# Kernel tuning notes

Measured on AMD Instinct MI355X. Metric: run time of the kernel, lower is better.

The kernel has to match this reference:

```python
import jax, jax.numpy as jnp
import numpy as np

MARGIN = 0.8
EPS = 1e-6  # torch F.pairwise_distance eps added to the difference


def setup_inputs() -> dict:
    key = jax.random.key(0)
    k1, k2, k3 = jax.random.split(key, 3)
    B, D = 8192, 128
    emb = jax.random.normal(k1, (B, D), dtype=jnp.float32)
    labels = jax.random.randint(k2, (B,), 0, 6)
    sbj = jax.random.randint(k3, (B,), 0, 16)
    return {"emb": emb, "labels": labels, "sbj": sbj}


def reference(emb, labels, sbj):
    B = emb.shape[0]
    # Squared pairwise distances (monotone in true distance -> same argmax/argmin)
    sq = jnp.sum(emb * emb, axis=1)
    d2 = sq[:, None] + sq[None, :] - 2.0 * (emb @ emb.T)  # [B, B]
    same_s = sbj[:, None] == sbj[None, :]
    same_l = labels[:, None] == labels[None, :]
    eye = jnp.eye(B, dtype=bool)
    pos_m = same_s & same_l & ~eye          # within-subject, same label, not self
    neg_m = same_s & ~same_l                # within-subject, different label
    valid = pos_m.any(axis=1) & neg_m.any(axis=1)
    p_idx = jnp.argmax(jnp.where(pos_m, d2, -jnp.inf), axis=1)  # hardest positive
    n_idx = jnp.argmin(jnp.where(neg_m, d2, jnp.inf), axis=1)   # hardest negative
    # TripletMarginLoss(p=2): pairwise_distance adds eps to the difference
    dap = jnp.linalg.norm(emb - emb[p_idx] + EPS, axis=1)
    dan = jnp.linalg.norm(emb - emb[n_idx] + EPS, axis=1)
    per = jnp.maximum(dap - dan + MARGIN, 0.0)
    cnt = jnp.sum(valid)
    loss = jnp.sum(jnp.where(valid, per, 0.0)) / jnp.maximum(cnt, 1)
    return jnp.where(cnt > 0, loss, 0.0)
```

## Files before the change

### kernel.cpp

```cpp
#include <hip/hip_runtime.h>
#include <math.h>
#include <limits.h>

#define D 128
#define NSUBJ 16
#define MAXN 640
#define MARGIN 0.8f
#define PRB 32
#define NPB 256
#define TI 16
#define TJ 64
#define NSTRIPE 32
#define NBLK (NSUBJ * NSTRIPE)

typedef __attribute__((ext_vector_type(8))) short bf16x8;
typedef __attribute__((ext_vector_type(4))) float f32x4;

static __device__ __forceinline__ short f2bf(float f) {
    union { float f; unsigned u; } v; v.f = f;
    unsigned r = v.u + 0x7FFF + ((v.u >> 16) & 1);
    return (short)(r >> 16);
}

__global__ __launch_bounds__(64) void hist_kernel(const int* __restrict__ sbj,
                                                  int* __restrict__ hist) {
    __shared__ int s_cnt[NSUBJ];
    const int t = threadIdx.x, bid = blockIdx.x;
    if (t < NSUBJ) s_cnt[t] = 0;
    __syncthreads();
    if (t < PRB) atomicAdd(&s_cnt[sbj[bid * PRB + t]], 1);
    __syncthreads();
    if (t < NSUBJ) hist[bid * NSUBJ + t] = s_cnt[t];
}

__global__ __launch_bounds__(256) void prep_kernel(
        const float* __restrict__ emb, const int* __restrict__ labels,
        const int* __restrict__ sbj, const int* __restrict__ hist,
        int* __restrict__ counts,
        int4* __restrict__ pmeta, short* __restrict__ ebf, int B) {
    __shared__ int s_cnt[NSUBJ], s_base[NSUBJ], s_slot[PRB];
    const int t = threadIdx.x, bid = blockIdx.x;
    if (t < NSUBJ) { s_cnt[t] = 0; s_base[t] = 0; }
    __syncthreads();
    {
        const int ss = t & 15, seg0 = (t >> 4) * 16;
        int part = 0;
        const int hi = min(bid, seg0 + 16);
        for (int b = seg0; b < hi; ++b) part += hist[b * NSUBJ + ss];
        if (part) atomicAdd(&s_base[ss], part);
    }
    int s = 0, mypos = 0;
    if (t < PRB) { s = sbj[bid * PRB + t]; mypos = atomicAdd(&s_cnt[s], 1); }
    __syncthreads();
    if (t < PRB) {
        int pos = s_base[s] + mypos;
        s_slot[t] = (pos < MAXN) ? (s * MAXN + pos) : -1;
    }
    if (bid == NPB - 1 && t < NSUBJ)
        counts[t] = s_base[t] + s_cnt[t];
    __syncthreads();
#pragma unroll
    for (int it = 0; it < (PRB * 16) / 256; ++it) {
        int lin = it * 256 + t;
        int row = lin >> 4, u = lin & 15;
        int i = bid * PRB + row;
        int slot = s_slot[row];
        const float4* rp = (const float4*)(emb + (size_t)i * D);
        float4 a0 = rp[u * 2], a1 = rp[u * 2 + 1];
        float ssq = 0.f;
        ssq = fmaf(a0.x, a0.x, ssq); ssq = fmaf(a0.y, a0.y, ssq);
        ssq = fmaf(a0.z, a0.z, ssq); ssq = fmaf(a0.w, a0.w, ssq);
        ssq = fmaf(a1.x, a1.x, ssq); ssq = fmaf(a1.y, a1.y, ssq);
        ssq = fmaf(a1.z, a1.z, ssq); ssq = fmaf(a1.w, a1.w, ssq);
#pragma unroll
        for (int off = 8; off > 0; off >>= 1) ssq += __shfl_down(ssq, off, 16);
        if (slot >= 0) {
            bf16x8 pk;
            pk[0] = f2bf(a0.x); pk[1] = f2bf(a0.y); pk[2] = f2bf(a0.z); pk[3] = f2bf(a0.w);
            pk[4] = f2bf(a1.x); pk[5] = f2bf(a1.y); pk[6] = f2bf(a1.z); pk[7] = f2bf(a1.w);
            *(bf16x8*)&ebf[(size_t)slot * D + u * 8] = pk;
            if (u == 0)
                pmeta[slot] = make_int4(labels[i], i, __float_as_int(ssq), 0);
        }
    }
}

#define LOADTILE(B0, B1, B2, B3, MI, ML, MS, JT)                         \
    do {                                                                 \
        int jl_ = (JT) * TJ + w * 16 + c, cl_ = min(jl_, n - 1);         \
        const short* rp_ = ebf + (size_t)(base + cl_) * D;               \
        B0 = *(const bf16x8*)&rp_[q * 8];                                \
        B1 = *(const bf16x8*)&rp_[32 + q * 8];                           \
        B2 = *(const bf16x8*)&rp_[64 + q * 8];                           \
        B3 = *(const bf16x8*)&rp_[96 + q * 8];                           \
        int4 m_ = pmeta[base + cl_];                                     \
        MI = (jl_ < n) ? m_.y : -1; ML = m_.x; MS = __int_as_float(m_.z);\
    } while (0)

#define STEP(B0, B1, B2, B3, MI, ML, MS)                                 \
    do {                                                                 \
        f32x4 acc = {0.f, 0.f, 0.f, 0.f};                                \
        acc = __builtin_amdgcn_mfma_f32_16x16x32_bf16(afr[0], B0, acc, 0, 0, 0); \
        acc = __builtin_amdgcn_mfma_f32_16x16x32_bf16(afr[1], B1, acc, 0, 0, 0); \
        acc = __builtin_amdgcn_mfma_f32_16x16x32_bf16(afr[2], B2, acc, 0, 0, 0); \
        acc = __builtin_amdgcn_mfma_f32_16x16x32_bf16(afr[3], B3, acc, 0, 0, 0); \
        if ((MI) >= 0) {                                                 \
            _Pragma("unroll")                                            \
            for (int r = 0; r < 4; ++r) {                                \
                float v = fmaf(-2.f, acc[r], (MS));                      \
                if ((ML) == li[r]) {                                     \
                    if ((MI) != gI[r] && v > vP[r]) { vP[r] = v; iP[r] = (MI); } \
                } else if (v < vN[r]) { vN[r] = v; iN[r] = (MI); }       \
            }                                                            \
        }                                                                \
    } while (0)

__global__ __launch_bounds__(256, 2) void triplet_kernel(
        const short* __restrict__ ebf, const int4* __restrict__ pmeta,
        const int* __restrict__ counts,
        float* __restrict__ bsum, int* __restrict__ bcnt) {
    const int bid = blockIdx.x, t = threadIdx.x;
    const int s = bid & 15;
    const int stripe = bid >> 4;
    const int base = s * MAXN;
    const int n = min(counts[s], MAXN);
    const int lane = t & 63, w = t >> 6, c = lane & 15, q = lane >> 4;

    __shared__ float svP[TI][4]; __shared__ int siP[TI][4];
    __shared__ float svN[TI][4]; __shared__ int siN[TI][4];

    float blockSum = 0.f; int blockCnt = 0;

    for (int i0 = stripe * TI; i0 < n; i0 += NSTRIPE * TI) {
        const int nrows = min(TI, n - i0);

        bf16x8 afr[4];
        {
            const short* ap = ebf + (size_t)(base + i0 + min(c, nrows - 1)) * D;
#pragma unroll
            for (int st = 0; st < 4; ++st)
                afr[st] = *(const bf16x8*)&ap[st * 32 + q * 8];
        }
        int li[4], gI[4];
#pragma unroll
        for (int r = 0; r < 4; ++r) {
            int row = q * 4 + r;
            if (row < nrows) { int4 m = pmeta[base + i0 + row]; li[r] = m.x; gI[r] = m.y; }
            else             { li[r] = INT_MIN; gI[r] = -1; }
        }

        float vP[4], vN[4]; int iP[4], iN[4];
#pragma unroll
        for (int r = 0; r < 4; ++r) {
            vP[r] = -INFINITY; iP[r] = -1;
            vN[r] =  INFINITY; iN[r] = -1;
        }

        const int ntiles = (n + TJ - 1) / TJ;
        bf16x8 b00, b01, b02, b03, b10, b11, b12, b13;
        bf16x8 b20, b21, b22, b23, b30, b31, b32, b33;
        int mi0 = -1, ml0 = INT_MIN, mi1 = -1, ml1 = INT_MIN;
        int mi2 = -1, ml2 = INT_MIN, mi3 = -1, ml3 = INT_MIN;
        float ms0 = 0.f, ms1 = 0.f, ms2 = 0.f, ms3 = 0.f;
        if (0 < ntiles) LOADTILE(b00, b01, b02, b03, mi0, ml0, ms0, 0);
        if (1 < ntiles) LOADTILE(b10, b11, b12, b13, mi1, ml1, ms1, 1);
        if (2 < ntiles) LOADTILE(b20, b21, b22, b23, mi2, ml2, ms2, 2);
        if (3 < ntiles) LOADTILE(b30, b31, b32, b33, mi3, ml3, ms3, 3);

        for (int jt = 0; jt < ntiles; jt += 4) {
            {
                bf16x8 c0 = b00, c1 = b01, c2 = b02, c3 = b03;
                int cmi = mi0, cml = ml0; float cms = ms0;
                if (jt + 4 < ntiles) LOADTILE(b00, b01, b02, b03, mi0, ml0, ms0, jt + 4);
                STEP(c0, c1, c2, c3, cmi, cml, cms);
            }
            if (jt + 1 < ntiles) {
                bf16x8 c0 = b10, c1 = b11, c2 = b12, c3 = b13;
                int cmi = mi1, cml = ml1; float cms = ms1;
                if (jt + 5 < ntiles) LOADTILE(b10, b11, b12, b13, mi1, ml1, ms1, jt + 5);
                STEP(c0, c1, c2, c3, cmi, cml, cms);
            }
            if (jt + 2 < ntiles) {
                bf16x8 c0 = b20, c1 = b21, c2 = b22, c3 = b23;
                int cmi = mi2, cml = ml2; float cms = ms2;
                if (jt + 6 < ntiles) LOADTILE(b20, b21, b22, b23, mi2, ml2, ms2, jt + 6);
                STEP(c0, c1, c2, c3, cmi, cml, cms);
            }
            if (jt + 3 < ntiles) {
                bf16x8 c0 = b30, c1 = b31, c2 = b32, c3 = b33;
                int cmi = mi3, cml = ml3; float cms = ms3;
                if (jt + 7 < ntiles) LOADTILE(b30, b31, b32, b33, mi3, ml3, ms3, jt + 7);
                STEP(c0, c1, c2, c3, cmi, cml, cms);
            }
        }

#pragma unroll
        for (int off = 8; off > 0; off >>= 1) {
#pragma unroll
            for (int r = 0; r < 4; ++r) {
                float ov = __shfl_down(vP[r], off, 16);
                int   oi = __shfl_down(iP[r], off, 16);
                if (ov > vP[r] || (ov == vP[r] && (unsigned)oi < (unsigned)iP[r])) {
                    vP[r] = ov; iP[r] = oi;
                }
                float on = __shfl_down(vN[r], off, 16);
                int   oj = __shfl_down(iN[r], off, 16);
                if (on < vN[r] || (on == vN[r] && (unsigned)oj < (unsigned)iN[r])) {
                    vN[r] = on; iN[r] = oj;
                }
            }
        }
        if (c == 0) {
#pragma unroll
            for (int r = 0; r < 4; ++r) {
                int row = q * 4 + r;
                svP[row][w] = vP[r]; siP[row][w] = iP[r];
                svN[row][w] = vN[r]; siN[row][w] = iN[r];
            }
        }
        __syncthreads();

        if (t < TI) {
            float bp = svP[t][0]; int ip = siP[t][0];
            float bn = svN[t][0]; int in_ = siN[t][0];
#pragma unroll
            for (int ww = 1; ww < 4; ++ww) {
                float o = svP[t][ww]; int oi = siP[t][ww];
                if (o > bp || (o == bp && (unsigned)oi < (unsigned)ip)) { bp = o; ip = oi; }
                float on = svN[t][ww]; int oj = siN[t][ww];
                if (on < bn || (on == bn && (unsigned)oj < (unsigned)in_)) { bn = on; in_ = oj; }
            }
            bool valid = (t < nrows) && (ip >= 0) && (in_ >= 0);
            float sqi = __int_as_float(pmeta[base + i0 + min(t, nrows - 1)].z);
            float per = 0.f;
            if (valid) {
                float dap = sqrtf(fmaxf(bp + sqi, 0.f));
                float dan = sqrtf(fmaxf(bn + sqi, 0.f));
                per = fmaxf(dap - dan + MARGIN, 0.f);
            }
            int vc = valid ? 1 : 0;
#pragma unroll
            for (int off = 8; off > 0; off >>= 1) {
                per += __shfl_down(per, off, 16);
                vc  += __shfl_down(vc,  off, 16);
            }
            if (t == 0) { blockSum += per; blockCnt += vc; }
        }
        if (i0 + NSTRIPE * TI < n) __syncthreads();
    }

    if (t == 0) { bsum[bid] = blockSum; bcnt[bid] = blockCnt; }
}

__global__ __launch_bounds__(256) void finalize_kernel(
        const float* __restrict__ bsum, const int* __restrict__ bcnt,
        float* __restrict__ out) {
    __shared__ float ssum[4]; __shared__ int scnt[4];
    const int t = threadIdx.x;
    float s = 0.f; int c = 0;
#pragma unroll
    for (int i = t; i < NBLK; i += 256) { s += bsum[i]; c += bcnt[i]; }
#pragma unroll
    for (int off = 32; off > 0; off >>= 1) {
        s += __shfl_down(s, off, 64);
        c += __shfl_down(c, off, 64);
    }
    if ((t & 63) == 0) { ssum[t >> 6] = s; scnt[t >> 6] = c; }
    __syncthreads();
    if (t == 0) {
        float S = ssum[0] + ssum[1] + ssum[2] + ssum[3];
        int   C = scnt[0] + scnt[1] + scnt[2] + scnt[3];
        out[0] = (C > 0) ? (S / (float)C) : 0.0f;
    }
}

extern "C" void kernel_launch(void* const* d_in, const int* in_sizes, int n_in,
                              void* d_out, int out_size, void* d_ws, size_t ws_size,
                              hipStream_t stream) {
    const float* emb    = (const float*)d_in[0];
    const int*   labels = (const int*)d_in[1];
    const int*   sbj    = (const int*)d_in[2];
    float*       out    = (float*)d_out;
    int B = in_sizes[1];

    char*  ws        = (char*)d_ws;
    int*   counts    = (int*)ws;
    float* bsum      = (float*)(ws + 256);
    int*   bcnt      = (int*)(ws + 256 + NBLK * sizeof(float));
    int*   hist      = (int*)(ws + 256 + 2 * NBLK * sizeof(int));
    size_t pmeta_off = (256 + 2 * (size_t)NBLK * sizeof(int)
                        + (size_t)NPB * NSUBJ * sizeof(int) + 255) & ~(size_t)255;
    int4*  pmeta     = (int4*)(ws + pmeta_off);
    size_t ebf_off   = (pmeta_off + (size_t)NSUBJ * MAXN * sizeof(int4) + 255) & ~(size_t)255;
    short* ebf       = (short*)(ws + ebf_off);

    hist_kernel<<<B / PRB, 64, 0, stream>>>(sbj, hist);
    prep_kernel<<<B / PRB, 256, 0, stream>>>(emb, labels, sbj, hist, counts,
                                             pmeta, ebf, B);
    triplet_kernel<<<NBLK, 256, 0, stream>>>(ebf, pmeta, counts, bsum, bcnt);
    finalize_kernel<<<1, 256, 0, stream>>>(bsum, bcnt, out);
}
```

Baseline: 91.61 us.

## Split column tiles across two blocks per row stripe and merge partial argmax/argmin in finalize

After: 112.8 us. 23.1% more time.

```diff
diff --git a/kernel.cpp b/kernel.cpp
--- a/kernel.cpp
+++ b/kernel.cpp
@@ -11,7 +11,9 @@
 #define TI 16
 #define TJ 64
 #define NSTRIPE 32
-#define NBLK (NSUBJ * NSTRIPE)
+#define NSPLIT 2
+#define NBLK (NSUBJ * NSTRIPE * NSPLIT)
+#define HROWS (NSUBJ * MAXN)
 
 typedef __attribute__((ext_vector_type(8))) short bf16x8;
 typedef __attribute__((ext_vector_type(4))) float f32x4;
@@ -115,13 +117,13 @@
         }                                                                \
     } while (0)
 
-__global__ __launch_bounds__(256, 2) void triplet_kernel(
+__global__ __launch_bounds__(256, 4) void triplet_kernel(
         const short* __restrict__ ebf, const int4* __restrict__ pmeta,
-        const int* __restrict__ counts,
-        float* __restrict__ bsum, int* __restrict__ bcnt) {
+        const int* __restrict__ counts, float4* __restrict__ parr) {
     const int bid = blockIdx.x, t = threadIdx.x;
     const int s = bid & 15;
-    const int stripe = bid >> 4;
+    const int stripe = (bid >> 4) & 31;
+    const int h = bid >> 9;
     const int base = s * MAXN;
     const int n = min(counts[s], MAXN);
     const int lane = t & 63, w = t >> 6, c = lane & 15, q = lane >> 4;
@@ -129,7 +131,10 @@
     __shared__ float svP[TI][4]; __shared__ int siP[TI][4];
     __shared__ float svN[TI][4]; __shared__ int siN[TI][4];
 
-    float blockSum = 0.f; int blockCnt = 0;
+    const int nt  = (n + TJ - 1) / TJ;
+    const int nt0 = (nt + 1) >> 1;
+    const int jt0 = h ? nt0 : 0;
+    const int jte = h ? nt : nt0;
 
     for (int i0 = stripe * TI; i0 < n; i0 += NSTRIPE * TI) {
         const int nrows = min(TI, n - i0);
@@ -156,40 +161,23 @@
             vN[r] =  INFINITY; iN[r] = -1;
         }
 
-        const int ntiles = (n + TJ - 1) / TJ;
         bf16x8 b00, b01, b02, b03, b10, b11, b12, b13;
-        bf16x8 b20, b21, b22, b23, b30, b31, b32, b33;
         int mi0 = -1, ml0 = INT_MIN, mi1 = -1, ml1 = INT_MIN;
-        int mi2 = -1, ml2 = INT_MIN, mi3 = -1, ml3 = INT_MIN;
-        float ms0 = 0.f, ms1 = 0.f, ms2 = 0.f, ms3 = 0.f;
-        if (0 < ntiles) LOADTILE(b00, b01, b02, b03, mi0, ml0, ms0, 0);
-        if (1 < ntiles) LOADTILE(b10, b11, b12, b13, mi1, ml1, ms1, 1);
-        if (2 < ntiles) LOADTILE(b20, b21, b22, b23, mi2, ml2, ms2, 2);
-        if (3 < ntiles) LOADTILE(b30, b31, b32, b33, mi3, ml3, ms3, 3);
-
-        for (int jt = 0; jt < ntiles; jt += 4) {
+        float ms0 = 0.f, ms1 = 0.f;
+        if (jt0 < jte)     LOADTILE(b00, b01, b02, b03, mi0, ml0, ms0, jt0);
+        if (jt0 + 1 < jte) LOADTILE(b10, b11, b12, b13, mi1, ml1, ms1, jt0 + 1);
+
+        for (int jt = jt0; jt < jte; jt += 2) {
             {
                 bf16x8 c0 = b00, c1 = b01, c2 = b02, c3 = b03;
                 int cmi = mi0, cml = ml0; float cms = ms0;
-                if (jt + 4 < ntiles) LOADTILE(b00, b01, b02, b03, mi0, ml0, ms0, jt + 4);
+                if (jt + 2 < jte) LOADTILE(b00, b01, b02, b03, mi0, ml0, ms0, jt + 2);
                 STEP(c0, c1, c2, c3, cmi, cml, cms);
             }
-            if (jt + 1 < ntiles) {
+            if (jt + 1 < jte) {
                 bf16x8 c0 = b10, c1 = b11, c2 = b12, c3 = b13;
                 int cmi = mi1, cml = ml1; float cms = ms1;
-                if (jt + 5 < ntiles) LOADTILE(b10, b11, b12, b13, mi1, ml1, ms1, jt + 5);
-                STEP(c0, c1, c2, c3, cmi, cml, cms);
-            }
-            if (jt + 2 < ntiles) {
-                bf16x8 c0 = b20, c1 = b21, c2 = b22, c3 = b23;
-                int cmi = mi2, cml = ml2; float cms = ms2;
-                if (jt + 6 < ntiles) LOADTILE(b20, b21, b22, b23, mi2, ml2, ms2, jt + 6);
-                STEP(c0, c1, c2, c3, cmi, cml, cms);
-            }
-            if (jt + 3 < ntiles) {
-                bf16x8 c0 = b30, c1 = b31, c2 = b32, c3 = b33;
-                int cmi = mi3, cml = ml3; float cms = ms3;
-                if (jt + 7 < ntiles) LOADTILE(b30, b31, b32, b33, mi3, ml3, ms3, jt + 7);
+                if (jt + 3 < jte) LOADTILE(b10, b11, b12, b13, mi1, ml1, ms1, jt + 3);
                 STEP(c0, c1, c2, c3, cmi, cml, cms);
             }
         }
@@ -230,47 +218,64 @@
                 float on = svN[t][ww]; int oj = siN[t][ww];
                 if (on < bn || (on == bn && (unsigned)oj < (unsigned)in_)) { bn = on; in_ = oj; }
             }
-            bool valid = (t < nrows) && (ip >= 0) && (in_ >= 0);
-            float sqi = __int_as_float(pmeta[base + i0 + min(t, nrows - 1)].z);
-            float per = 0.f;
-            if (valid) {
+            if (t < nrows) {
+                float4 v;
+                v.x = bp; v.y = __int_as_float(ip);
+                v.z = bn; v.w = __int_as_float(in_);
+                parr[(size_t)h * HROWS + base + i0 + t] = v;
+            }
+        }
+        if (i0 + NSTRIPE * TI < n) __syncthreads();
+    }
+}
+
+__global__ __launch_bounds__(1024) void finalize_kernel(
+        const float4* __restrict__ parr, const int4* __restrict__ pmeta,
+        const int* __restrict__ counts, float* __restrict__ out) {
+    __shared__ float fs[16]; __shared__ int fc[16];
+    const int t = threadIdx.x;
+    float sum = 0.f; int cnt = 0;
+    for (int s = 0; s < NSUBJ; ++s) {
+        const int ns = min(counts[s], MAXN);
+        for (int r = t; r < ns; r += 1024) {
+            const int slot = s * MAXN + r;
+            float4 a = parr[slot];
+            float4 b = parr[HROWS + slot];
+            float bp = a.x; int ip = __float_as_int(a.y);
+            {
+                float o = b.x; int oi = __float_as_int(b.z == b.z ? b.y : b.y);
+                oi = __float_as_int(b.y);
+                if (o > bp || (o == bp && (unsigned)oi < (unsigned)ip)) { bp = o; ip = oi; }
+            }
+            float bn = a.z; int in_ = __float_as_int(a.w);
+            {
+                float o = b.z; int oi = __float_as_int(b.w);
+                if (o < bn || (o == bn && (unsigned)oi < (unsigned)in_)) { bn = o; in_ = oi; }
+            }
+            if (ip >= 0 && in_ >= 0) {
+                float sqi = __int_as_float(pmeta[slot].z);
                 float dap = sqrtf(fmaxf(bp + sqi, 0.f));
                 float dan = sqrtf(fmaxf(bn + sqi, 0.f));
-                per = fmaxf(dap - dan + MARGIN, 0.f);
-            }
-            int vc = valid ? 1 : 0;
-#pragma unroll
-            for (int off = 8; off > 0; off >>= 1) {
-                per += __shfl_down(per, off, 16);
-                vc  += __shfl_down(vc,  off, 16);
-            }
-            if (t == 0) { blockSum += per; blockCnt += vc; }
-        }
-        if (i0 + NSTRIPE * TI < n) __syncthreads();
-    }
-
-    if (t == 0) { bsum[bid] = blockSum; bcnt[bid] = blockCnt; }
-}
-
-__global__ __launch_bounds__(256) void finalize_kernel(
-        const float* __restrict__ bsum, const int* __restrict__ bcnt,
-        float* __restrict__ out) {
-    __shared__ float ssum[4]; __shared__ int scnt[4];
-    const int t = threadIdx.x;
-    float s = 0.f; int c = 0;
-#pragma unroll
-    for (int i = t; i < NBLK; i += 256) { s += bsum[i]; c += bcnt[i]; }
+                sum += fmaxf(dap - dan + MARGIN, 0.f);
+                cnt += 1;
+            }
+        }
+    }
 #pragma unroll
     for (int off = 32; off > 0; off >>= 1) {
-        s += __shfl_down(s, off, 64);
-        c += __shfl_down(c, off, 64);
-    }
-    if ((t & 63) == 0) { ssum[t >> 6] = s; scnt[t >> 6] = c; }
-    __syncthreads();
-    if (t == 0) {
-        float S = ssum[0] + ssum[1] + ssum[2] + ssum[3];
-        int   C = scnt[0] + scnt[1] + scnt[2] + scnt[3];
-        out[0] = (C > 0) ? (S / (float)C) : 0.0f;
+        sum += __shfl_down(sum, off, 64);
+        cnt += __shfl_down(cnt, off, 64);
+    }
+    if ((t & 63) == 0) { fs[t >> 6] = sum; fc[t >> 6] = cnt; }
+    __syncthreads();
+    if (t < 16) {
+        float s2 = fs[t]; int c2 = fc[t];
+#pragma unroll
+        for (int off = 8; off > 0; off >>= 1) {
+            s2 += __shfl_down(s2, off, 16);
+            c2 += __shfl_down(c2, off, 16);
+        }
+        if (t == 0) out[0] = (c2 > 0) ? (s2 / (float)c2) : 0.0f;
     }
 }
 
@@ -285,18 +290,17 @@
 
     char*  ws        = (char*)d_ws;
     int*   counts    = (int*)ws;
-    float* bsum      = (float*)(ws + 256);
-    int*   bcnt      = (int*)(ws + 256 + NBLK * sizeof(float));
-    int*   hist      = (int*)(ws + 256 + 2 * NBLK * sizeof(int));
-    size_t pmeta_off = (256 + 2 * (size_t)NBLK * sizeof(int)
-                        + (size_t)NPB * NSUBJ * sizeof(int) + 255) & ~(size_t)255;
+    int*   hist      = (int*)(ws + 256);
+    size_t parr_off  = (256 + (size_t)NPB * NSUBJ * sizeof(int) + 255) & ~(size_t)255;
+    float4* parr     = (float4*)(ws + parr_off);
+    size_t pmeta_off = (parr_off + 2 * (size_t)HROWS * sizeof(float4) + 255) & ~(size_t)255;
     int4*  pmeta     = (int4*)(ws + pmeta_off);
-    size_t ebf_off   = (pmeta_off + (size_t)NSUBJ * MAXN * sizeof(int4) + 255) & ~(size_t)255;
+    size_t ebf_off   = (pmeta_off + (size_t)HROWS * sizeof(int4) + 255) & ~(size_t)255;
     short* ebf       = (short*)(ws + ebf_off);
 
     hist_kernel<<<B / PRB, 64, 0, stream>>>(sbj, hist);
     prep_kernel<<<B / PRB, 256, 0, stream>>>(emb, labels, sbj, hist, counts,
                                              pmeta, ebf, B);
-    triplet_kernel<<<NBLK, 256, 0, stream>>>(ebf, pmeta, counts, bsum, bcnt);
-    finalize_kernel<<<1, 256, 0, stream>>>(bsum, bcnt, out);
-}
+    triplet_kernel<<<NBLK, 256, 0, stream>>>(ebf, pmeta, counts, parr);
+    finalize_kernel<<<1, 1024, 0, stream>>>(parr, pmeta, counts, out);
+}
```

## Fuse final reduction into triplet kernel with flag-based cross-block wait

Applied to the files above, without the earlier changes.

New measurement: 93.04 us. Within noise of the previous version (+1.6%).

```diff
diff --git a/kernel.cpp b/kernel.cpp
--- a/kernel.cpp
+++ b/kernel.cpp
@@ -36,10 +36,11 @@
 __global__ __launch_bounds__(256) void prep_kernel(
         const float* __restrict__ emb, const int* __restrict__ labels,
         const int* __restrict__ sbj, const int* __restrict__ hist,
-        int* __restrict__ counts,
+        int* __restrict__ counts, int* __restrict__ bcnt,
         int4* __restrict__ pmeta, short* __restrict__ ebf, int B) {
     __shared__ int s_cnt[NSUBJ], s_base[NSUBJ], s_slot[PRB];
     const int t = threadIdx.x, bid = blockIdx.x;
+    if (t < 2) bcnt[bid * 2 + t] = 0;
     if (t < NSUBJ) { s_cnt[t] = 0; s_base[t] = 0; }
     __syncthreads();
     {
@@ -118,7 +119,8 @@
 __global__ __launch_bounds__(256, 2) void triplet_kernel(
         const short* __restrict__ ebf, const int4* __restrict__ pmeta,
         const int* __restrict__ counts,
-        float* __restrict__ bsum, int* __restrict__ bcnt) {
+        float* __restrict__ bsum, int* __restrict__ bcnt,
+        float* __restrict__ out) {
     const int bid = blockIdx.x, t = threadIdx.x;
     const int s = bid & 15;
     const int stripe = bid >> 4;
@@ -128,6 +130,7 @@
 
     __shared__ float svP[TI][4]; __shared__ int siP[TI][4];
     __shared__ float svN[TI][4]; __shared__ int siN[TI][4];
+    __shared__ float fsum[4]; __shared__ int fcnt[4];
 
     float blockSum = 0.f; int blockCnt = 0;
 
@@ -249,28 +252,37 @@
         if (i0 + NSTRIPE * TI < n) __syncthreads();
     }
 
-    if (t == 0) { bsum[bid] = blockSum; bcnt[bid] = blockCnt; }
-}
-
-__global__ __launch_bounds__(256) void finalize_kernel(
-        const float* __restrict__ bsum, const int* __restrict__ bcnt,
-        float* __restrict__ out) {
-    __shared__ float ssum[4]; __shared__ int scnt[4];
-    const int t = threadIdx.x;
-    float s = 0.f; int c = 0;
-#pragma unroll
-    for (int i = t; i < NBLK; i += 256) { s += bsum[i]; c += bcnt[i]; }
-#pragma unroll
-    for (int off = 32; off > 0; off >>= 1) {
-        s += __shfl_down(s, off, 64);
-        c += __shfl_down(c, off, 64);
-    }
-    if ((t & 63) == 0) { ssum[t >> 6] = s; scnt[t >> 6] = c; }
-    __syncthreads();
     if (t == 0) {
-        float S = ssum[0] + ssum[1] + ssum[2] + ssum[3];
-        int   C = scnt[0] + scnt[1] + scnt[2] + scnt[3];
-        out[0] = (C > 0) ? (S / (float)C) : 0.0f;
+        __hip_atomic_store(&bsum[bid], blockSum,
+                           __ATOMIC_RELAXED, __HIP_MEMORY_SCOPE_AGENT);
+        asm volatile("s_waitcnt vmcnt(0)" ::: "memory");
+        __hip_atomic_store(&bcnt[bid], blockCnt + 1,
+                           __ATOMIC_RELAXED, __HIP_MEMORY_SCOPE_AGENT);
+    }
+
+    if (bid == 0) {
+        float s2 = 0.f; int c2 = 0;
+        for (int i = t; i < NBLK; i += 256) {
+            int v;
+            while ((v = __hip_atomic_load(&bcnt[i], __ATOMIC_RELAXED,
+                                          __HIP_MEMORY_SCOPE_AGENT)) == 0)
+                __builtin_amdgcn_s_sleep(8);
+            c2 += v - 1;
+            s2 += __hip_atomic_load(&bsum[i], __ATOMIC_RELAXED,
+                                    __HIP_MEMORY_SCOPE_AGENT);
+        }
+#pragma unroll
+        for (int off = 32; off > 0; off >>= 1) {
+            s2 += __shfl_down(s2, off, 64);
+            c2 += __shfl_down(c2, off, 64);
+        }
+        if ((t & 63) == 0) { fsum[t >> 6] = s2; fcnt[t >> 6] = c2; }
+        __syncthreads();
+        if (t == 0) {
+            float S = fsum[0] + fsum[1] + fsum[2] + fsum[3];
+            int   C = fcnt[0] + fcnt[1] + fcnt[2] + fcnt[3];
+            out[0] = (C > 0) ? (S / (float)C) : 0.0f;
+        }
     }
 }
 
@@ -296,7 +308,6 @@
 
     hist_kernel<<<B / PRB, 64, 0, stream>>>(sbj, hist);
     prep_kernel<<<B / PRB, 256, 0, stream>>>(emb, labels, sbj, hist, counts,
-                                             pmeta, ebf, B);
-    triplet_kernel<<<NBLK, 256, 0, stream>>>(ebf, pmeta, counts, bsum, bcnt);
-    finalize_kernel<<<1, 256, 0, stream>>>(bsum, bcnt, out);
-}
+                                             bcnt, pmeta, ebf, B);
+    triplet_kernel<<<NBLK, 256, 0, stream>>>(ebf, pmeta, counts, bsum, bcnt, out);
+}
```

## Stage column tiles into swizzled LDS via async global_load_lds double buffering

Applied to the files above, without the earlier changes.

Result: faster. 86.27 us (-5.8%).

```diff
diff --git a/kernel.cpp b/kernel.cpp
--- a/kernel.cpp
+++ b/kernel.cpp
@@ -20,6 +20,12 @@
     union { float f; unsigned u; } v; v.f = f;
     unsigned r = v.u + 0x7FFF + ((v.u >> 16) & 1);
     return (short)(r >> 16);
+}
+
+static __device__ __forceinline__ void gload_lds16(const void* g, void* l) {
+    __builtin_amdgcn_global_load_lds(
+        (const __attribute__((address_space(1))) void*)g,
+        (__attribute__((address_space(3))) void*)l, 16, 0, 0);
 }
 
 __global__ __launch_bounds__(64) void hist_kernel(const int* __restrict__ sbj,
@@ -85,34 +91,16 @@
     }
 }
 
-#define LOADTILE(B0, B1, B2, B3, MI, ML, MS, JT)                         \
-    do {                                                                 \
-        int jl_ = (JT) * TJ + w * 16 + c, cl_ = min(jl_, n - 1);         \
-        const short* rp_ = ebf + (size_t)(base + cl_) * D;               \
-        B0 = *(const bf16x8*)&rp_[q * 8];                                \
-        B1 = *(const bf16x8*)&rp_[32 + q * 8];                           \
-        B2 = *(const bf16x8*)&rp_[64 + q * 8];                           \
-        B3 = *(const bf16x8*)&rp_[96 + q * 8];                           \
-        int4 m_ = pmeta[base + cl_];                                     \
-        MI = (jl_ < n) ? m_.y : -1; ML = m_.x; MS = __int_as_float(m_.z);\
-    } while (0)
-
-#define STEP(B0, B1, B2, B3, MI, ML, MS)                                 \
-    do {                                                                 \
-        f32x4 acc = {0.f, 0.f, 0.f, 0.f};                                \
-        acc = __builtin_amdgcn_mfma_f32_16x16x32_bf16(afr[0], B0, acc, 0, 0, 0); \
-        acc = __builtin_amdgcn_mfma_f32_16x16x32_bf16(afr[1], B1, acc, 0, 0, 0); \
-        acc = __builtin_amdgcn_mfma_f32_16x16x32_bf16(afr[2], B2, acc, 0, 0, 0); \
-        acc = __builtin_amdgcn_mfma_f32_16x16x32_bf16(afr[3], B3, acc, 0, 0, 0); \
-        if ((MI) >= 0) {                                                 \
-            _Pragma("unroll")                                            \
-            for (int r = 0; r < 4; ++r) {                                \
-                float v = fmaf(-2.f, acc[r], (MS));                      \
-                if ((ML) == li[r]) {                                     \
-                    if ((MI) != gI[r] && v > vP[r]) { vP[r] = v; iP[r] = (MI); } \
-                } else if (v < vN[r]) { vN[r] = v; iN[r] = (MI); }       \
-            }                                                            \
-        }                                                                \
+#define STAGE(BUF, JT)                                                    \
+    do {                                                                  \
+        const char* ts_ = (const char*)ebf + ((size_t)(base + (JT) * TJ)) * 256; \
+        _Pragma("unroll")                                                 \
+        for (int ii_ = 0; ii_ < 4; ++ii_) {                               \
+            int lin_ = ((w * 4 + ii_) * 64 + lane) * 16;                  \
+            int row_ = lin_ >> 8;                                         \
+            gload_lds16(ts_ + (lin_ ^ ((row_ & 7) << 4)),                 \
+                        ldsB + (BUF) * (TJ * 256) + (w * 4 + ii_) * 1024);\
+        }                                                                 \
     } while (0)
 
 __global__ __launch_bounds__(256, 2) void triplet_kernel(
@@ -126,8 +114,16 @@
     const int n = min(counts[s], MAXN);
     const int lane = t & 63, w = t >> 6, c = lane & 15, q = lane >> 4;
 
+    __shared__ char ldsB[2 * TJ * 256];
+    __shared__ char ldsM[MAXN * 16];
     __shared__ float svP[TI][4]; __shared__ int siP[TI][4];
     __shared__ float svN[TI][4]; __shared__ int siN[TI][4];
+
+    const int ntiles = (n + TJ - 1) / TJ;
+
+    for (int r = w; r < ntiles; r += 4)
+        gload_lds16((const char*)(pmeta + base + r * 64) + lane * 16,
+                    ldsM + r * 1024);
 
     float blockSum = 0.f; int blockCnt = 0;
 
@@ -156,42 +152,49 @@
             vN[r] =  INFINITY; iN[r] = -1;
         }
 
-        const int ntiles = (n + TJ - 1) / TJ;
-        bf16x8 b00, b01, b02, b03, b10, b11, b12, b13;
-        bf16x8 b20, b21, b22, b23, b30, b31, b32, b33;
-        int mi0 = -1, ml0 = INT_MIN, mi1 = -1, ml1 = INT_MIN;
-        int mi2 = -1, ml2 = INT_MIN, mi3 = -1, ml3 = INT_MIN;
-        float ms0 = 0.f, ms1 = 0.f, ms2 = 0.f, ms3 = 0.f;
-        if (0 < ntiles) LOADTILE(b00, b01, b02, b03, mi0, ml0, ms0, 0);
-        if (1 < ntiles) LOADTILE(b10, b11, b12, b13, mi1, ml1, ms1, 1);
-        if (2 < ntiles) LOADTILE(b20, b21, b22, b23, mi2, ml2, ms2, 2);
-        if (3 < ntiles) LOADTILE(b30, b31, b32, b33, mi3, ml3, ms3, 3);
-
-        for (int jt = 0; jt < ntiles; jt += 4) {
+        STAGE(0, 0);
+        if (1 < ntiles) STAGE(1, 1);
+        int cur = 0;
+
+        for (int jt = 0; jt < ntiles; ++jt) {
+            if (jt + 1 < ntiles) asm volatile("s_waitcnt vmcnt(4)" ::: "memory");
+            else                 asm volatile("s_waitcnt vmcnt(0)" ::: "memory");
+            __builtin_amdgcn_sched_barrier(0);
+            __builtin_amdgcn_s_barrier();
+            __builtin_amdgcn_sched_barrier(0);
+
             {
-                bf16x8 c0 = b00, c1 = b01, c2 = b02, c3 = b03;
-                int cmi = mi0, cml = ml0; float cms = ms0;
-                if (jt + 4 < ntiles) LOADTILE(b00, b01, b02, b03, mi0, ml0, ms0, jt + 4);
-                STEP(c0, c1, c2, c3, cmi, cml, cms);
-            }
-            if (jt + 1 < ntiles) {
-                bf16x8 c0 = b10, c1 = b11, c2 = b12, c3 = b13;
-                int cmi = mi1, cml = ml1; float cms = ms1;
-                if (jt + 5 < ntiles) LOADTILE(b10, b11, b12, b13, mi1, ml1, ms1, jt + 5);
-                STEP(c0, c1, c2, c3, cmi, cml, cms);
-            }
-            if (jt + 2 < ntiles) {
-                bf16x8 c0 = b20, c1 = b21, c2 = b22, c3 = b23;
-                int cmi = mi2, cml = ml2; float cms = ms2;
-                if (jt + 6 < ntiles) LOADTILE(b20, b21, b22, b23, mi2, ml2, ms2, jt + 6);
-                STEP(c0, c1, c2, c3, cmi, cml, cms);
-            }
-            if (jt + 3 < ntiles) {
-                bf16x8 c0 = b30, c1 = b31, c2 = b32, c3 = b33;
-                int cmi = mi3, cml = ml3; float cms = ms3;
-                if (jt + 7 < ntiles) LOADTILE(b30, b31, b32, b33, mi3, ml3, ms3, jt + 7);
-                STEP(c0, c1, c2, c3, cmi, cml, cms);
-            }
+                const char* bb = ldsB + cur * (TJ * 256);
+                const int lr = w * 16 + c, swz = (lr & 7) << 4;
+                bf16x8 f0 = *(const bf16x8*)(bb + lr * 256 + ((  0 + q * 16) ^ swz));
+                bf16x8 f1 = *(const bf16x8*)(bb + lr * 256 + (( 64 + q * 16) ^ swz));
+                bf16x8 f2 = *(const bf16x8*)(bb + lr * 256 + ((128 + q * 16) ^ swz));
+                bf16x8 f3 = *(const bf16x8*)(bb + lr * 256 + ((192 + q * 16) ^ swz));
+                const int jl = jt * TJ + lr;
+                int4 m = *(const int4*)(ldsM + jl * 16);
+                const int MI = (jl < n) ? m.y : -1;
+                const int ML = m.x; const float MS = __int_as_float(m.z);
+
+                f32x4 acc = {0.f, 0.f, 0.f, 0.f};
+                acc = __builtin_amdgcn_mfma_f32_16x16x32_bf16(afr[0], f0, acc, 0, 0, 0);
+                acc = __builtin_amdgcn_mfma_f32_16x16x32_bf16(afr[1], f1, acc, 0, 0, 0);
+                acc = __builtin_amdgcn_mfma_f32_16x16x32_bf16(afr[2], f2, acc, 0, 0, 0);
+                acc = __builtin_amdgcn_mfma_f32_16x16x32_bf16(afr[3], f3, acc, 0, 0, 0);
+                if (MI >= 0) {
+#pragma unroll
+                    for (int r = 0; r < 4; ++r) {
+                        float v = fmaf(-2.f, acc[r], MS);
+                        if (ML == li[r]) {
+                            if (MI != gI[r] && v > vP[r]) { vP[r] = v; iP[r] = MI; }
+                        } else if (v < vN[r]) { vN[r] = v; iN[r] = MI; }
+                    }
+                }
+            }
+
+            __builtin_amdgcn_s_barrier();
+            __builtin_amdgcn_sched_barrier(0);
+            if (jt + 2 < ntiles) STAGE(cur, jt + 2);
+            cur ^= 1;
         }
 
 #pragma unroll
@@ -231,7 +234,8 @@
                 if (on < bn || (on == bn && (unsigned)oj < (unsigned)in_)) { bn = on; in_ = oj; }
             }
             bool valid = (t < nrows) && (ip >= 0) && (in_ >= 0);
-            float sqi = __int_as_float(pmeta[base + i0 + min(t, nrows - 1)].z);
+            float sqi = __int_as_float(
+                ((const int4*)(ldsM + (i0 + min(t, nrows - 1)) * 16))->z);
             float per = 0.f;
             if (valid) {
                 float dap = sqrtf(fmaxf(bp + sqi, 0.f));
```
